# Kernel optimization log

Measured on AMD Instinct MI355X. Metric: run time of the kernel, lower is better.

The kernel has to match this reference:

```python
import jax, jax.numpy as jnp
import numpy as np

N = 48
E = N * (N - 1)
H_LSTM = 32
EPS = 20.0

def _conv1d(x, w, b):
    # x: [B, Cin, L], w: [Cout, Cin, K] -> [B, Cout, L], 'same' padding
    y = jax.lax.conv_general_dilated(x, w, window_strides=(1,), padding='SAME',
                                     dimension_numbers=('NCH', 'OIH', 'NCH'))
    return y + b[None, :, None]

def _map(M, x):
    # map_features: linear map along dim 0 (gather for n_to_e one-hot rows,
    # incidence-sum scatter for e_to_n). M: [O, I], x: [I, ...] -> [O, ...]
    return jnp.tensordot(M, x, axes=1)

def _node_cnn(x, adj, layers, final):
    # graph conv stack: neighbor mix (adj along dim 0) + conv1d over node axis + relu
    nl = len(layers)
    for i, (w, b) in enumerate(layers):
        x = _conv1d(_map(adj, x), w, b)
        if not (final and i == nl - 1):
            x = jax.nn.relu(x)
    return x

def _node_lstm(x, mem, adj, w, b):
    # mem = cat([c, h], dim=1); gates from conv over adj-mixed cat([x, h])
    H = mem.shape[1] // 2
    c, h = mem[:, :H], mem[:, H:]
    gates = _conv1d(_map(adj, jnp.concatenate([x, h], axis=1)), w, b)
    i, f, g, o = jnp.split(gates, 4, axis=1)
    c2 = jax.nn.sigmoid(f) * c + jax.nn.sigmoid(i) * jnp.tanh(g)
    h2 = jax.nn.sigmoid(o) * jnp.tanh(c2)
    return jnp.concatenate([c2, h2], axis=1)

def _forward(bi, bij, msgi, msgj, v, nmem0, emem0, neadj, eeadj,
             e_to_n0, e_to_n1, n_to_e0, n_to_e1, decoding, params):
    fm, efm, nlstm, elstm, pp, epp = params
    n = bi.shape[0]
    e = bij.shape[0]
    # map_node_feature_to_edge
    bi_g1 = _map(n_to_e0, bi)   # [E,1,N]
    bi_g2 = _map(n_to_e1, bi)   # [E,1,N]
    # softmax (logsumexp) message computation over bij [E,1,N,N]
    cmsgi = jax.nn.logsumexp((bi_g2[:, :, None, :] + bij) * EPS, axis=3) / EPS  # [E,1,N]
    cmsgj = jax.nn.logsumexp((bi_g1[:, :, :, None] + bij) * EPS, axis=2) / EPS  # [E,1,N]
    ncmsgi = _map(e_to_n0, cmsgi)
    ncmsgj = _map(e_to_n1, cmsgj)
    nnmsgi = _map(e_to_n0, msgi)
    nnmsgj = _map(e_to_n1, msgj)
    # partial_feature (detached in original)
    dec_mat = jax.nn.one_hot(decoding, n, dtype=bi.dtype)        # [N,N]
    xi = _map(n_to_e0, dec_mat)[:, :, None]                      # [E,N,1]
    xj = _map(n_to_e1, dec_mat)[:, None, :]                      # [E,1,N]
    ep = bij.reshape(e, n, n)
    f1 = jax.lax.stop_gradient(_map(e_to_n0, (ep * xi).sum(axis=1)).reshape(n, 1, n))
    f2 = jax.lax.stop_gradient(_map(e_to_n1, (ep * xj).sum(axis=2)).reshape(n, 1, n))
    node_feature = jnp.concatenate([bi, bi + v, nnmsgi, nnmsgj, ncmsgi, ncmsgj, f1, f2], axis=1)  # [N,8,N]
    edge_feature = jnp.concatenate([msgi, msgj, cmsgi, cmsgj, bi_g1, bi_g2], axis=1)              # [E,6,N]
    nfeat = _node_cnn(node_feature, neadj, fm, False)   # [N,32,N]
    efeat = _node_cnn(edge_feature, eeadj, efm, False)  # [E,32,N]
    ntoe1, ntoe2 = _map(n_to_e0, nfeat), _map(n_to_e1, nfeat)
    eton1, eton2 = _map(e_to_n0, efeat), _map(e_to_n1, efeat)
    nfeat = jnp.concatenate([nfeat, eton1, eton2], axis=1)  # [N,96,N]
    efeat = jnp.concatenate([efeat, ntoe1, ntoe2], axis=1)  # [E,96,N]
    nmem_new = _node_lstm(nfeat, nmem0, neadj, nlstm[0], nlstm[1])  # [N,64,N]
    emem_new = _node_lstm(efeat, emem0, eeadj, elstm[0], elstm[1])  # [E,64,N]
    nfeat = nmem_new[:, H_LSTM:]   # h part
    efeat = emem_new[:, H_LSTM:]
    ntoe1, ntoe2 = _map(n_to_e0, nfeat), _map(n_to_e1, nfeat)
    eton1, eton2 = _map(e_to_n0, efeat), _map(e_to_n1, efeat)
    nfeat = jnp.concatenate([nfeat, eton1, eton2], axis=1)
    efeat = jnp.concatenate([efeat, ntoe1, ntoe2], axis=1)
    efeat = _node_cnn(efeat, eeadj, epp, True)   # [E,2,N]
    nfeat = _node_cnn(nfeat, neadj, pp, True)    # [N,1,N]
    nmsgi = efeat[:, 0:1] + 0.5 * cmsgi - msgi
    nmsgj = efeat[:, 1:2] + 0.5 * cmsgj - msgj
    nv = nfeat.mean(axis=0, keepdims=True)       # [1,1,N]
    v_out = v + nv
    bij_out = bij - nmsgi.reshape(e, 1, n, 1) - nmsgj.reshape(e, 1, 1, n)
    bi_out = bi + _map(e_to_n0, nmsgi) + _map(e_to_n1, nmsgj) - nv
    msgi_out = msgi + nmsgi
    msgj_out = msgj + nmsgj
    # get_current_dual (softmax=True)
    cdual = (v_out.sum()
             + jax.nn.logsumexp(bi_out.reshape(-1, n) * EPS, axis=1).sum() / EPS
             + jax.nn.logsumexp(bij_out.reshape(-1, n * n) * EPS, axis=1).sum() / EPS)
    return bi_out, bij_out, msgi_out, msgj_out, v_out, cdual, nmem_new, emem_new, f1, f2

def setup_inputs() -> dict:
    key = jax.random.key(0)
    ks = jax.random.split(key, 16)
    ii, jj = np.meshgrid(np.arange(N), np.arange(N), indexing='ij')
    mask = ii != jj
    src, dst = ii[mask], jj[mask]  # [E] complete directed graph
    eye = np.eye(N, dtype=np.float32)
    n_to_e0 = jnp.asarray(eye[src])  # [E,N] one-hot gather
    n_to_e1 = jnp.asarray(eye[dst])
    e_to_n0 = n_to_e0.T              # [N,E] incidence scatter-sum
    e_to_n1 = n_to_e1.T
    def glorot(k, shape):
        fan_in = shape[1] * shape[2]
        return jax.random.normal(k, shape, jnp.float32) / np.sqrt(fan_in)
    pk = jax.random.split(ks[15], 20)
    return dict(
        bi=jax.random.normal(ks[0], (N, 1, N), jnp.float32),
        bij=jax.random.normal(ks[1], (E, 1, N, N), jnp.float32),
        msgi=jnp.zeros((E, 1, N), jnp.float32),
        msgj=jnp.zeros((E, 1, N), jnp.float32),
        v=jnp.zeros((1, 1, N), jnp.float32),
        nmem0=jnp.zeros((N, 2 * H_LSTM, N), jnp.float32),
        emem0=jnp.zeros((E, 2 * H_LSTM, N), jnp.float32),
        neadj=jax.random.uniform(ks[2], (N, N), jnp.float32) / N,
        eeadj=jax.random.uniform(ks[3], (E, E), jnp.float32) / E,
        e_to_n0=e_to_n0, e_to_n1=e_to_n1, n_to_e0=n_to_e0, n_to_e1=n_to_e1,
        decoding=jax.random.randint(ks[4], (N,), 0, N),
        fm_w0=glorot(pk[0], (32, 8, 3)), fm_b0=jnp.zeros((32,), jnp.float32),
        fm_w1=glorot(pk[1], (32, 32, 3)), fm_b1=jnp.zeros((32,), jnp.float32),
        efm_w0=glorot(pk[2], (32, 6, 3)), efm_b0=jnp.zeros((32,), jnp.float32),
        efm_w1=glorot(pk[3], (32, 32, 3)), efm_b1=jnp.zeros((32,), jnp.float32),
        nlstm_w=glorot(pk[4], (128, 128, 3)), nlstm_b=jnp.zeros((128,), jnp.float32),
        elstm_w=glorot(pk[5], (128, 128, 3)), elstm_b=jnp.zeros((128,), jnp.float32),
        pp_w0=glorot(pk[6], (16, 96, 3)), pp_b0=jnp.zeros((16,), jnp.float32),
        pp_w1=glorot(pk[7], (1, 16, 3)), pp_b1=jnp.zeros((1,), jnp.float32),
        epp_w0=glorot(pk[8], (16, 96, 3)), epp_b0=jnp.zeros((16,), jnp.float32),
        epp_w1=glorot(pk[9], (2, 16, 3)), epp_b1=jnp.zeros((2,), jnp.float32),
    )

def reference(bi, bij, msgi, msgj, v, nmem0, emem0, neadj, eeadj,
              e_to_n0, e_to_n1, n_to_e0, n_to_e1, decoding,
              fm_w0, fm_b0, fm_w1, fm_b1, efm_w0, efm_b0, efm_w1, efm_b1,
              nlstm_w, nlstm_b, elstm_w, elstm_b,
              pp_w0, pp_b0, pp_w1, pp_b1, epp_w0, epp_b0, epp_w1, epp_b1):
    params = ([(fm_w0, fm_b0), (fm_w1, fm_b1)],
              [(efm_w0, efm_b0), (efm_w1, efm_b1)],
              (nlstm_w, nlstm_b), (elstm_w, elstm_b),
              [(pp_w0, pp_b0), (pp_w1, pp_b1)],
              [(epp_w0, epp_b0), (epp_w1, epp_b1)])
    return _forward(bi, bij, msgi, msgj, v, nmem0, emem0, neadj, eeadj,
                    e_to_n0, e_to_n1, n_to_e0, n_to_e1, decoding, params)
```

## Files before the change

kernel.cpp:

```cpp
#include <hip/hip_runtime.h>
#include <cstdint>
#include <cstddef>

#define EE 2256
#define EP 2304

typedef __attribute__((ext_vector_type(8))) short bf16x8;
typedef __attribute__((ext_vector_type(4))) float f32x4;

__device__ __forceinline__ unsigned short f2b(float f){
  unsigned u = __builtin_bit_cast(unsigned, f);
  u += 0x7fffu + ((u>>16)&1u);
  return (unsigned short)(u>>16);
}
__device__ __forceinline__ float b2f(unsigned short h){
  unsigned u = ((unsigned)h)<<16; return __builtin_bit_cast(float, u);
}
__device__ __forceinline__ float sigm(float x){ return 1.f/(1.f+__expf(-x)); }
__device__ __forceinline__ float tanhfast(float x){ return 1.f - 2.f/(__expf(2.f*x)+1.f); }

__device__ __forceinline__ int xcd_swz(int bid, int nwg){
  int xcd = bid & 7, idx = bid >> 3;
  int q = nwg >> 3, r = nwg & 7;
  return (xcd < r ? xcd*(q+1) : r*(q+1) + (xcd-r)*q) + idx;
// ... 80 lines not shown
                              float* ncmi, float* ncmj, float* nnmi, float* nnmj,
                              float* o_f1, float* o_f2){
  int i = blockIdx.x; int tid = threadIdx.x;
  __shared__ float red[5][6][48];
  int mg = tid / 48;
  int w  = tid - mg*48;
  if (mg < 5){
    int dc = dec[i];
    float a1=0,a2=0,a3=0,a4=0,s1=0,s2=0;
    for (int m=mg; m<47; m+=5){
      int e1 = i*47+m;
      a1 += cmi[e1*48+w]; a3 += msgi[e1*48+w];
      s1 += bij[(size_t)e1*2304 + dc*48 + w];
      int j = m + (m>=i); int e2 = j*47 + i - (i>j);
      a2 += cmj[e2*48+w]; a4 += msgj[e2*48+w];
      s2 += bij[(size_t)e2*2304 + w*48 + dc];
    }
    red[mg][0][w]=a1; red[mg][1][w]=a2; red[mg][2][w]=a3;
    red[mg][3][w]=a4; red[mg][4][w]=s1; red[mg][5][w]=s2;
  }
  __syncthreads();
  if (tid < 48){
    float a1=0,a2=0,a3=0,a4=0,s1=0,s2=0;
    for (int g=0; g<5; g++){
      a1+=red[g][0][tid]; a2+=red[g][1][tid]; a3+=red[g][2][tid];
      a4+=red[g][3][tid]; s1+=red[g][4][tid]; s2+=red[g][5][tid];
    }
    ncmi[i*48+tid]=a1; ncmj[i*48+tid]=a2; nnmi[i*48+tid]=a3; nnmj[i*48+tid]=a4;
    o_f1[i*48+tid]=s1; o_f2[i*48+tid]=s2;
  }
}

__global__ void gm_build_x6(const float* __restrict__ msgi, const float* __restrict__ msgj,
                            const float* __restrict__ cmi, const float* __restrict__ cmj,
                            const float* __restrict__ bi, unsigned short* __restrict__ x6){
  int idx = blockIdx.x*256 + threadIdx.x;
  if (idx >= 288*EP) return;
  int row = idx / EP, e = idx - row*EP;
  int w = row / 6, c = row - w*6;
  unsigned short val = 0;
  if (e < EE){
    int s = e/47, m = e-s*47, d = m + (m>=s);
    float x;
    switch(c){
      case 0: x = msgi[e*48+w]; break;
      case 1: x = msgj[e*48+w]; break;
      case 2: x = cmi[e*48+w]; break;
      case 3: x = cmj[e*48+w]; break;
      case 4: x = bi[s*48+w]; break;
      default: x = bi[d*48+w]; break;
    }
    val = f2b(x);
  }
  x6[idx] = val;
}

__global__ void gm_fill_x128_hi(const float* __restrict__ emem0, const float* __restrict__ nfeat,
                                unsigned short* __restrict__ x128){
  int idx = blockIdx.x*256 + threadIdx.x;
  if (idx >= 96*EP) return;
  int q = idx/EP; int c = 32 + q; int e = idx - q*EP;
  if (e >= EE){ for (int w=0;w<48;w++) x128[(size_t)(w*128+c)*EP + e] = 0; return; }
  int s=e/47, m=e-s*47, d=m+(m>=s);
  const float* srcrow;
  if (c < 64)      srcrow = nfeat + ((size_t)s*32 + (c-32))*48;
  else if (c < 96) srcrow = nfeat + ((size_t)d*32 + (c-64))*48;
  else             srcrow = emem0 + ((size_t)e*64 + (c-64))*48;
  #pragma unroll
  for (int w4=0; w4<12; w4++){
    float4 xv = *(const float4*)(srcrow + w4*4);
    x128[(size_t)((w4*4+0)*128+c)*EP + e] = f2b(xv.x);
    x128[(size_t)((w4*4+1)*128+c)*EP + e] = f2b(xv.y);
    x128[(size_t)((w4*4+2)*128+c)*EP + e] = f2b(xv.z);
    x128[(size_t)((w4*4+3)*128+c)*EP + e] = f2b(xv.w);
  }
}

__global__ __launch_bounds__(256) void gm_map_gemm(
    const unsigned short* __restrict__ A, const unsigned short* __restrict__ BT,
    unsigned short* __restrict__ ypad, float* __restrict__ outf,
    const float* __restrict__ bias, int nrow, int Nvalid, int Cch, int Cslab,
    int do_relu, int f32_out)
{
  __shared__ __align__(16) unsigned short lA[2][128*32];
  __shared__ __align__(16) unsigned short lB[2][128*32];
  const int tid = threadIdx.x;
  const int lane = tid & 63, wid = tid >> 6;
  const int swz = xcd_swz(blockIdx.x, gridDim.x);
  const int m0 = (swz % nrow) * 128;
  const int n0 = (swz / nrow) * 128;
  const int wm = wid >> 1, wn = wid & 1;
  f32x4 acc[4][4];
  #pragma unroll
  for (int i=0;i<4;i++){
    #pragma unroll
    for (int j=0;j<4;j++) acc[i][j] = f32x4{0.f,0.f,0.f,0.f};
  }
  const int srow = (lane>>2), scol = (lane&3);

  auto STAGE = [&](int ks, int b){
    #pragma unroll
    for (int q=0;q<2;q++){
      int chunk = wid*2+q;
      int row = chunk*16 + srow;
      int off = (scol*16) ^ (((row>>1)&3)<<4);
      glds16((const char*)A  + (size_t)(m0+row)*(EP*2) + ks*64 + off, (char*)lA[b] + chunk*1024);
      glds16((const char*)BT + (size_t)(n0+row)*(EP*2) + ks*64 + off, (char*)lB[b] + chunk*1024);
    }
  };
  auto COMPUTE = [&](int b){
    bf16x8 af[4], bfr[4];
    #pragma unroll
    for (int mi=0;mi<4;mi++){
      int row = wm*64 + mi*16 + (lane&15);
      int off = ((lane>>4)*16) ^ (((row>>1)&3)<<4);
      af[mi] = *(const bf16x8*)((const char*)lA[b] + row*64 + off);
    }
    #pragma unroll
    for (int ni=0;ni<4;ni++){
      int row = wn*64 + ni*16 + (lane&15);
      int off = ((lane>>4)*16) ^ (((row>>1)&3)<<4);
      bfr[ni] = *(const bf16x8*)((const char*)lB[b] + row*64 + off);
    }
    #pragma unroll
    for (int mi=0;mi<4;mi++){
      #pragma unroll
      for (int ni=0;ni<4;ni++)
        acc[mi][ni] = __builtin_amdgcn_mfma_f32_16x16x32_bf16(af[mi], bfr[ni], acc[mi][ni], 0,0,0);
    }
  };

  STAGE(0, 0);
  __syncthreads();
  int cur = 0;
  for (int ks = 0; ks < EP/32; ++ks){
    if (ks+1 < EP/32) STAGE(ks+1, cur^1);
    COMPUTE(cur);
    __syncthreads();
    cur ^= 1;
  }
  #pragma unroll
  for (int mi=0;mi<4;mi++){
    int ebase = m0 + wm*64 + mi*16 + (lane>>4)*4;
    #pragma unroll
    for (int ni=0;ni<4;ni++){
      int c = n0 + wn*64 + ni*16 + (lane&15);
      if (c >= Nvalid) continue;
      int w = c / Cch, ci = c - w*Cch;
      float bv = bias ? bias[ci] : 0.f;
      #pragma unroll
      for (int r=0;r<4;r++){
        int e = ebase + r;
        if (e >= EE) continue;
        float x = acc[mi][ni][r] + bv;
        if (do_relu) x = fmaxf(x, 0.f);
        if (f32_out) outf[(size_t)e*Nvalid + c] = x;
        else ypad[((size_t)e*50 + 1 + w)*Cslab + ci] = f2b(x);
      }
    }
  }
}

__global__ __launch_bounds__(256) void gm_map_sk(
    const unsigned short* __restrict__ A, const unsigned short* __restrict__ BT,
    float* __restrict__ pbuf, int nrow, int ncol, int S, int kspan)
{
  __shared__ __align__(16) unsigned short lA[2][128*32];
  __shared__ __align__(16) unsigned short lB[2][128*32];
  const int tid = threadIdx.x;
  const int lane = tid & 63, wid = tid >> 6;
  const int swz = xcd_swz(blockIdx.x, gridDim.x);
  const int ntile = nrow*ncol;
  const int sp = swz / ntile;
  const int tile = swz - sp*ntile;
  const int m0 = (tile % nrow) * 128;
  const int n0 = (tile / nrow) * 128;
  const int Npad = ncol*128;
  const int k0 = sp*kspan, k1 = k0 + kspan;
  const int wm = wid >> 1, wn = wid & 1;
  f32x4 acc[4][4];
  #pragma unroll
  for (int i=0;i<4;i++){
    #pragma unroll
    for (int j=0;j<4;j++) acc[i][j] = f32x4{0.f,0.f,0.f,0.f};
  }
  const int srow = (lane>>2), scol = (lane&3);

  auto STAGE = [&](int ks, int b){
    #pragma unroll
    for (int q=0;q<2;q++){
      int chunk = wid*2+q;
      int row = chunk*16 + srow;
      int off = (scol*16) ^ (((row>>1)&3)<<4);
      glds16((const char*)A  + (size_t)(m0+row)*(EP*2) + ks*64 + off, (char*)lA[b] + chunk*1024);
      glds16((const char*)BT + (size_t)(n0+row)*(EP*2) + ks*64 + off, (char*)lB[b] + chunk*1024);
    }
  };
  auto COMPUTE = [&](int b){
    bf16x8 af[4], bfr[4];
    #pragma unroll
    for (int mi=0;mi<4;mi++){
      int row = wm*64 + mi*16 + (lane&15);
      int off = ((lane>>4)*16) ^ (((row>>1)&3)<<4);
      af[mi] = *(const bf16x8*)((const char*)lA[b] + row*64 + off);
    }
    #pragma unroll
    for (int ni=0;ni<4;ni++){
      int row = wn*64 + ni*16 + (lane&15);
      int off = ((lane>>4)*16) ^ (((row>>1)&3)<<4);
      bfr[ni] = *(const bf16x8*)((const char*)lB[b] + row*64 + off);
    }
    #pragma unroll
    for (int mi=0;mi<4;mi++){
      #pragma unroll
      for (int ni=0;ni<4;ni++)
        acc[mi][ni] = __builtin_amdgcn_mfma_f32_16x16x32_bf16(af[mi], bfr[ni], acc[mi][ni], 0,0,0);
    }
  };

  STAGE(k0, 0);
  __syncthreads();
  int cur = 0;
  for (int ks = k0; ks < k1; ++ks){
    if (ks+1 < k1) STAGE(ks+1, cur^1);
    COMPUTE(cur);
    __syncthreads();
    cur ^= 1;
  }
  float* pb = pbuf + (size_t)sp*2304*Npad;
  #pragma unroll
  for (int mi=0;mi<4;mi++){
    int ebase = m0 + wm*64 + mi*16 + (lane>>4)*4;
    #pragma unroll
    for (int ni=0;ni<4;ni++){
      int c = n0 + wn*64 + ni*16 + (lane&15);
      #pragma unroll
      for (int r=0;r<4;r++)
        pb[(size_t)(ebase+r)*Npad + c] = acc[mi][ni][r];
    }
  }
}

__global__ void gm_sk_fin(const float* __restrict__ pbuf, unsigned short* __restrict__ ypad,
                          float* __restrict__ outf, const float* __restrict__ bias,
                          int S, int Npad, int Nvalid, int Cch, int Cslab, int do_relu, int f32_out){
  int idx = blockIdx.x*256 + threadIdx.x;
  if (idx >= EE*Nvalid) return;
  int e = idx / Nvalid, c = idx - e*Nvalid;
  float s = 0.f;
  for (int p=0;p<S;p++) s += pbuf[(size_t)p*2304*Npad + (size_t)e*Npad + c];
  int w = c / Cch, ci = c - w*Cch;
  if (bias) s += bias[ci];
  if (do_relu) s = fmaxf(s, 0.f);
  if (f32_out) outf[(size_t)e*Nvalid + c] = s;
  else ypad[((size_t)e*50 + 1 + w)*Cslab + ci] = f2b(s);
}

template<int BM>
__global__ __launch_bounds__(256) void gm_conv_gemm(
    const unsigned short* __restrict__ Wp, const unsigned short* __restrict__ ypad,
    unsigned short* __restrict__ outT, const float* __restrict__ bias,
    int Cch, int KPT, int Kpad, int Co, int Ct, int do_relu)
{
  constexpr int MI = (BM==128)?4:((BM==32)?2:1);
  constexpr int NI = (BM==128)?4:2;
  __shared__ __align__(16) unsigned short lA[2][BM*32];
  __shared__ __align__(16) unsigned short lB[2][128*32];
  const int tid = threadIdx.x, lane = tid&63, wid = tid>>6;
  const int swz = xcd_swz(blockIdx.x, 864);
  const int e0 = (swz / 48) * 128;
  const int w  = swz % 48;
  const int rowb = (BM==128)? (wid>>1)*64 : 0;
  const int colb = (BM==128)? (wid&1)*64 : wid*32;
  f32x4 acc[MI][NI];
  #pragma unroll
  for (int i=0;i<MI;i++){
    #pragma unroll
    for (int j=0;j<NI;j++) acc[i][j] = f32x4{0.f,0.f,0.f,0.f};
  }
  const int srow=(lane>>2), scol=(lane&3);
  const int ksteps = Kpad/32;

  auto STAGE = [&](int ks, int b){
    for (int c = wid; c < BM/16; c += 4){
      int row = c*16 + srow;
      int off = (scol*16) ^ (((row>>1)&3)<<4);
      glds16((const char*)Wp + (size_t)row*(Kpad*2) + ks*64 + off, (char*)lA[b] + c*1024);
    }
    for (int c = wid; c < 8; c += 4){
      int row = c*16 + srow;
      int off = (scol*16) ^ (((row>>1)&3)<<4);
      int kg = ks*32 + (off>>1);
      int t = kg / KPT;
      int ci = kg - t*KPT;
      int e = e0 + row;
      const char* src;
      if (t < 3 && e < EE) src = (const char*)ypad + ((size_t)(e*50 + w + t)*Cch + ci)*2;
      else                 src = (const char*)ypad;
      glds16(src, (char*)lB[b] + c*1024);
    }
  };
  auto COMPUTE = [&](int b){
    bf16x8 af[MI], bfr[NI];
    #pragma unroll
    for (int mi=0;mi<MI;mi++){
      int row = rowb + mi*16 + (lane&15);
      int off = ((lane>>4)*16) ^ (((row>>1)&3)<<4);
      af[mi] = *(const bf16x8*)((const char*)lA[b] + row*64 + off);
    }
    #pragma unroll
    for (int ni=0;ni<NI;ni++){
      int row = colb + ni*16 + (lane&15);
      int off = ((lane>>4)*16) ^ (((row>>1)&3)<<4);
      bfr[ni] = *(const bf16x8*)((const char*)lB[b] + row*64 + off);
    }
    #pragma unroll
    for (int mi=0;mi<MI;mi++){
      #pragma unroll
      for (int ni=0;ni<NI;ni++)
        acc[mi][ni] = __builtin_amdgcn_mfma_f32_16x16x32_bf16(af[mi], bfr[ni], acc[mi][ni], 0,0,0);
    }
  };

  STAGE(0, 0);
  __syncthreads();
  int cur = 0;
  for (int ks=0; ks<ksteps; ++ks){
    if (ks+1 < ksteps) STAGE(ks+1, cur^1);
    COMPUTE(cur);
    __syncthreads();
    cur ^= 1;
  }
  #pragma unroll
  for (int mi=0;mi<MI;mi++){
    #pragma unroll
    for (int ni=0;ni<NI;ni++){
      int m = colb + ni*16 + (lane&15);
      int e = e0 + m;
      if (e >= EE) continue;
      #pragma unroll
      for (int r=0;r<4;r++){
        int co = rowb + mi*16 + (lane>>4)*4 + r;
        if (co >= Co) continue;
        float x = acc[mi][ni][r] + (bias ? bias[co] : 0.f);
        if (do_relu) x = fmaxf(x, 0.f);
        outT[((size_t)(w*Ct + co))*EP + e] = f2b(x);
      }
    }
  }
}

__global__ void gm_build_nf(const float* __restrict__ bi, const float* __restrict__ v,
                            const float* __restrict__ nnmi, const float* __restrict__ nnmj,
                            const float* __restrict__ ncmi, const float* __restrict__ ncmj,
                            const float* __restrict__ f1, const float* __restrict__ f2,
                            float* __restrict__ nf){
  int idx = blockIdx.x*256+threadIdx.x;
  if (idx >= 48*8*48) return;
  int i = idx/(8*48); int rem = idx - i*(8*48); int c = rem/48; int w = rem-c*48;
  int iw = i*48+w;
  float x;
  switch(c){
    case 0: x=bi[iw]; break;
    case 1: x=bi[iw]+v[w]; break;
    case 2: x=nnmi[iw]; break;
    case 3: x=nnmj[iw]; break;
    case 4: x=ncmi[iw]; break;
    case 5: x=ncmj[iw]; break;
    case 6: x=f1[iw]; break;
    default: x=f2[iw]; break;
  }
  nf[idx]=x;
}

__global__ void gm_nmap(const float* __restrict__ adj, const float* __restrict__ X,
                        float* __restrict__ Y, int C){
  int idx = blockIdx.x*256 + threadIdx.x;
  int tot = 48*C*48;
  if (idx >= tot) return;
  int i = idx/(C*48); int rem = idx - i*(C*48);
  float s=0.f;
  for (int j=0;j<48;j++) s += adj[i*48+j]*X[(size_t)j*C*48 + rem];
  Y[idx]=s;
}

__global__ void gm_nconv(const float* __restrict__ X, const float* __restrict__ wgt,
                         const float* __restrict__ bias, float* __restrict__ Y,
                         int Cin, int Co, int relu){
  int idx = blockIdx.x*256 + threadIdx.x;
  int tot = 48*Co*48;
  if (idx >= tot) return;
  int i = idx/(Co*48); int rem = idx - i*(Co*48); int co = rem/48; int w = rem-co*48;
  float s = bias[co];
  const float* xb = X + (size_t)i*Cin*48;
  const float* wb = wgt + (size_t)co*Cin*3;
  for (int ci=0; ci<Cin; ++ci){
    float w0 = wb[ci*3], w1 = wb[ci*3+1], w2 = wb[ci*3+2];
    const float* xr = xb + ci*48;
    if (w > 0) s += xr[w-1]*w0;
    s += xr[w]*w1;
    if (w < 47) s += xr[w+1]*w2;
  }
  if (relu) s = fmaxf(s, 0.f);
  Y[idx] = s;
}

__global__ __launch_bounds__(256) void gm_nconv_lstm(const float* __restrict__ X,
    const float* __restrict__ wgt, const float* __restrict__ bias,
    const float* __restrict__ nmem0, float* __restrict__ o_nmem, float* __restrict__ nfeat2){
  int idx = blockIdx.x*256 + threadIdx.x;
  if (idx >= 48*32*48) return;
  int i = idx/(32*48); int rem = idx - i*(32*48); int ch = rem/48; int w = rem-ch*48;
  const float* xb = X + (size_t)i*128*48;
  float s0=bias[ch], s1=bias[32+ch], s2=bias[64+ch], s3=bias[96+ch];
  for (int ci=0; ci<128; ++ci){
    const float* xr = xb + ci*48;
    float xm = (w>0)? xr[w-1] : 0.f;
    float xc = xr[w];
    float xp = (w<47)? xr[w+1] : 0.f;
    const float* wb0 = wgt + ((size_t)ch*128+ci)*3;
    const float* wb1 = wgt + ((size_t)(32+ch)*128+ci)*3;
    const float* wb2 = wgt + ((size_t)(64+ch)*128+ci)*3;
    const float* wb3 = wgt + ((size_t)(96+ch)*128+ci)*3;
    s0 += xm*wb0[0]+xc*wb0[1]+xp*wb0[2];
    s1 += xm*wb1[0]+xc*wb1[1]+xp*wb1[2];
    s2 += xm*wb2[0]+xc*wb2[1]+xp*wb2[2];
    s3 += xm*wb3[0]+xc*wb3[1]+xp*wb3[2];
  }
  float c = nmem0[((size_t)i*64+ch)*48+w];
  float c2 = sigm(s1)*c + sigm(s0)*tanhfast(s2);
  float h2 = sigm(s3)*tanhfast(c2);
  o_nmem[((size_t)i*64+ch)*48+w] = c2;
  o_nmem[((size_t)i*64+32+ch)*48+w] = h2;
  nfeat2[((size_t)i*32+ch)*48+w] = h2;
}

__global__ __launch_bounds__(256) void gm_eton_x128(const unsigned short* __restrict__ x128,
                                                    float* __restrict__ xn){
  int row = blockIdx.x;
  int w = row >> 5, cc = row & 31;
  __shared__ float L[2256];
  const unsigned short* src = x128 + (size_t)(w*128 + cc)*EP;
  for (int t=threadIdx.x; t<2256; t+=256) L[t] = b2f(src[t]);
  __syncthreads();
  int tid = threadIdx.x;
  if (tid < 48){
    int i = tid; float s=0.f;
    for (int m=0;m<47;m++) s += L[i*47+m];
    xn[((size_t)i*128 + 32 + cc)*48 + w] = s;
  } else if (tid >= 64 && tid < 112){
    int i = tid-64; float s=0.f;
    for (int m=0;m<47;m++){
      int j = m + (m>=i);
      s += L[j*47 + i - (i>j)];
    }
    xn[((size_t)i*128 + 64 + cc)*48 + w] = s;
  }
}

__global__ void gm_xnode_copy(const float* __restrict__ nfeat, const float* __restrict__ nmem0,
                              float* __restrict__ xn){
  int idx = blockIdx.x*256+threadIdx.x;
  if (idx >= 48*64*48) return;
  int i = idx/(64*48); int rem = idx - i*(64*48); int c = rem/48; int w = rem-c*48;
  if (c < 32) xn[((size_t)i*128 + c)*48 + w] = nfeat[((size_t)i*32+c)*48+w];
  else        xn[((size_t)i*128 + 96 + (c-32))*48 + w] = nmem0[((size_t)i*64 + 32 + (c-32))*48 + w];
}

__global__ __launch_bounds__(256) void gm_elstm_pw(const unsigned short* __restrict__ gatesT,
                                                   const float* __restrict__ emem0,
                                                   float* __restrict__ o_emem){
  int bid = blockIdx.x;
  int e4 = bid / 6, chunk = bid - e4*6;
  int cw = chunk*256 + threadIdx.x;
  int ch = cw / 48, w = cw - ch*48;
  int ebase = e4*4;
  const unsigned short* g0 = gatesT + (size_t)(w*128 + ch)*EP + ebase;
  ushort4 vi = *(const ushort4*)(g0);
  ushort4 vf = *(const ushort4*)(g0 + (size_t)32*EP);
  ushort4 vg = *(const ushort4*)(g0 + (size_t)64*EP);
  ushort4 vo = *(const ushort4*)(g0 + (size_t)96*EP);
  const unsigned short* pi = (const unsigned short*)&vi;
  const unsigned short* pf = (const unsigned short*)&vf;
  const unsigned short* pg = (const unsigned short*)&vg;
  const unsigned short* po = (const unsigned short*)&vo;
  #pragma unroll
  for (int r=0;r<4;r++){
    int e = ebase + r;
    float gi = b2f(pi[r]), gf = b2f(pf[r]), gg = b2f(pg[r]), go = b2f(po[r]);
    float c  = emem0[((size_t)e*64 + ch)*48 + w];
    float c2 = sigm(gf)*c + sigm(gi)*tanhfast(gg);
    float h2 = sigm(go)*tanhfast(c2);
    o_emem[((size_t)e*64 + ch)*48 + w] = c2;
    o_emem[((size_t)e*64 + 32+ch)*48 + w] = h2;
  }
}

__global__ __launch_bounds__(256) void gm_eton_h(const float* __restrict__ o_emem,
                                                 float* __restrict__ x2){
  int row = blockIdx.x; int w = row >> 5, cc = row & 31;
  __shared__ float L[2256];
  for (int t=threadIdx.x; t<2256; t+=256)
    L[t] = o_emem[((size_t)t*64 + 32 + cc)*48 + w];
  __syncthreads();
  int tid = threadIdx.x;
  if (tid < 48){
    int i=tid; float s=0.f;
    for (int m=0;m<47;m++) s += L[i*47+m];
    x2[((size_t)i*96 + 32 + cc)*48 + w] = s;
  } else if (tid>=64 && tid<112){
    int i=tid-64; float s=0.f;
    for (int m=0;m<47;m++){ int j=m+(m>=i); s += L[j*47 + i - (i>j)]; }
    x2[((size_t)i*96 + 64 + cc)*48 + w] = s;
  }
}

__global__ void gm_x2_copy(const float* __restrict__ nfeat2, float* __restrict__ x2){
// ... 69 lines not shown
    float x = src[idx] - ri[r] - rj[c];
    dst[idx] = x; v[q] = x; mx = fmaxf(mx, x);
  }
  for (int o=1;o<64;o<<=1) mx = fmaxf(mx, __shfl_xor(mx, o, 64));
  int lane = tid&63, w4 = tid>>6;
  if (lane==0) red[w4] = mx;
  __syncthreads();
  mx = fmaxf(fmaxf(red[0],red[1]),fmaxf(red[2],red[3]));
  float s = 0.f;
  #pragma unroll
  for (int q=0;q<9;q++) s += __expf((v[q]-mx)*20.f);
  for (int o=1;o<64;o<<=1) s += __shfl_xor(s, o, 64);
  if (lane==0) red[4+w4] = s;
  __syncthreads();
  if (tid==0){
    float t = red[4]+red[5]+red[6]+red[7];
    lse_e[e] = mx + __logf(t)*(1.f/20.f);
  }
}

__global__ void gm_biout(const float* __restrict__ bi, const float* __restrict__ nmi,
                         const float* __restrict__ nmj, const float* __restrict__ nv,
                         float* __restrict__ o_bi, float* __restrict__ lse_n){
  int i = blockIdx.x; int w = threadIdx.x;
  float val = -1e30f;
  if (w < 48){
    float s = 0.f;
    for (int m=0;m<47;m++){
      int e1 = i*47+m;
      s += nmi[e1*48+w];
      int j = m + (m>=i);
      int e2 = j*47 + i - (i>j);
      s += nmj[e2*48+w];
    }
    val = bi[i*48+w] + s - nv[w];
    o_bi[i*48+w] = val;
  }
  float mx = val;
  for (int o=1;o<64;o<<=1) mx = fmaxf(mx, __shfl_xor(mx, o, 64));
  float ex = (w<48)? __expf((val-mx)*20.f) : 0.f;
  for (int o=1;o<64;o<<=1) ex += __shfl_xor(ex, o, 64);
  if (w==0) lse_n[i] = mx + __logf(ex)*(1.f/20.f);
}

__global__ void gm_cdual(const float* __restrict__ lse_e, const float* __restrict__ lse_n,
                         const float* __restrict__ vout, float* __restrict__ out){
  int tid = threadIdx.x;
  float s = 0.f;
  for (int i=tid;i<EE;i+=256) s += lse_e[i];
  if (tid<48) s += lse_n[tid] + vout[tid];
  __shared__ float red[4];
  for (int o=1;o<64;o<<=1) s += __shfl_xor(s,o,64);
  if ((tid&63)==0) red[tid>>6]=s;
  __syncthreads();
  if (tid==0) out[0] = red[0]+red[1]+red[2]+red[3];
}

static constexpr size_t A256v(size_t x){ return (x+255)&~(size_t)255; }
static constexpr size_t OFF_EEADJ = 0;
static constexpr size_t OFF_X6T   = A256v(OFF_EEADJ + (size_t)EP*EP*2);
static constexpr size_t OFF_X32T  = A256v(OFF_X6T  + (size_t)384*EP*2);
static constexpr size_t OFF_X128T = A256v(OFF_X32T + (size_t)1536*EP*2);
static constexpr size_t OFF_YP6   = A256v(OFF_X128T + (size_t)6144*EP*2);
static constexpr size_t OFF_YP32  = A256v(OFF_YP6  + (size_t)EE*50*8*2);
static constexpr size_t OFF_YP128 = A256v(OFF_YP32 + (size_t)EE*50*32*2);
static constexpr size_t OFF_YP16  = A256v(OFF_YP128 + (size_t)EE*50*128*2);
static constexpr size_t OFF_ZEND  = A256v(OFF_YP16 + (size_t)EE*50*16*2 + 256);
static constexpr size_t OFF_XPP   = OFF_YP128;
static constexpr size_t OFF_SKP   = OFF_YP128;
static constexpr size_t OFF_WC0 = OFF_ZEND;
static constexpr size_t OFF_WC1 = A256v(OFF_WC0 + 32*32*2);
static constexpr size_t OFF_WCL = A256v(OFF_WC1 + 32*96*2);
static constexpr size_t OFF_WP0 = A256v(OFF_WCL + 128*384*2);
static constexpr size_t OFF_WP1 = A256v(OFF_WP0 + 16*288*2);
static constexpr size_t OFF_CMI = A256v(OFF_WP1 + 16*64*2);
static constexpr size_t OFF_CMJ = A256v(OFF_CMI + (size_t)EE*48*4);
static constexpr size_t OFF_NMI = A256v(OFF_CMJ + (size_t)EE*48*4);
static constexpr size_t OFF_NMJ = A256v(OFF_NMI + (size_t)EE*48*4);
static constexpr size_t OFF_EFPP= A256v(OFF_NMJ + (size_t)EE*48*4);
static constexpr size_t OFF_LSEE= A256v(OFF_EFPP + (size_t)EE*96*4);
static constexpr size_t OFF_LSEN= A256v(OFF_LSEE + EE*4);
static constexpr size_t OFF_NV  = A256v(OFF_LSEN + 48*4);
static constexpr size_t OFF_NF  = A256v(OFF_NV + 48*4);
static constexpr size_t OFF_NT1 = A256v(OFF_NF + (size_t)48*8*48*4);
static constexpr size_t OFF_NT2 = A256v(OFF_NT1 + (size_t)48*128*48*4);
static constexpr size_t OFF_NFEAT = A256v(OFF_NT2 + (size_t)48*128*48*4);
static constexpr size_t OFF_NFEAT2= A256v(OFF_NFEAT + (size_t)48*32*48*4);
static constexpr size_t OFF_XN  = A256v(OFF_NFEAT2 + (size_t)48*32*48*4);
static constexpr size_t OFF_NFPP= A256v(OFF_XN + (size_t)48*128*48*4);
static constexpr size_t OFF_NAC = A256v(OFF_NFPP + (size_t)48*48*4);

extern "C" void kernel_launch(void* const* d_in, const int* in_sizes, int n_in,
                              void* d_out, int out_size, void* d_ws, size_t ws_size,
                              hipStream_t stream) {
  const float* bi    = (const float*)d_in[0];
  const float* bij   = (const float*)d_in[1];
  const float* msgi  = (const float*)d_in[2];
  const float* msgj  = (const float*)d_in[3];
  const float* v_in  = (const float*)d_in[4];
  const float* nmem0 = (const float*)d_in[5];
  const float* emem0 = (const float*)d_in[6];
  const float* neadj = (const float*)d_in[7];
  const float* eeadj = (const float*)d_in[8];
  const int*   dec   = (const int*)d_in[13];
  const float* fm_w0 = (const float*)d_in[14]; const float* fm_b0 = (const float*)d_in[15];
  const float* fm_w1 = (const float*)d_in[16]; const float* fm_b1 = (const float*)d_in[17];
  const float* efm_w0= (const float*)d_in[18]; const float* efm_b0= (const float*)d_in[19];
  const float* efm_w1= (const float*)d_in[20]; const float* efm_b1= (const float*)d_in[21];
  const float* nl_w  = (const float*)d_in[22]; const float* nl_b  = (const float*)d_in[23];
  const float* el_w  = (const float*)d_in[24]; const float* el_b  = (const float*)d_in[25];
  const float* pp_w0 = (const float*)d_in[26]; const float* pp_b0 = (const float*)d_in[27];
  const float* pp_w1 = (const float*)d_in[28]; const float* pp_b1 = (const float*)d_in[29];
  const float* epp_w0= (const float*)d_in[30]; const float* epp_b0= (const float*)d_in[31];
  const float* epp_w1= (const float*)d_in[32]; const float* epp_b1= (const float*)d_in[33];

  char* ws = (char*)d_ws;
  unsigned short* eeadjb = (unsigned short*)(ws + OFF_EEADJ);
  unsigned short* x6t    = (unsigned short*)(ws + OFF_X6T);
  unsigned short* x32t   = (unsigned short*)(ws + OFF_X32T);
  unsigned short* x128t  = (unsigned short*)(ws + OFF_X128T);
  unsigned short* z1t    = x32t;
  unsigned short* z2t    = x6t;
  unsigned short* gatesT = x128t;
  unsigned short* yp6    = (unsigned short*)(ws + OFF_YP6);
  unsigned short* yp32   = (unsigned short*)(ws + OFF_YP32);
  unsigned short* yp128  = (unsigned short*)(ws + OFF_YP128);
  unsigned short* yp16   = (unsigned short*)(ws + OFF_YP16);
  unsigned short* xpp    = (unsigned short*)(ws + OFF_XPP);
  float*          skp    = (float*)(ws + OFF_SKP);
  unsigned short* wc0 = (unsigned short*)(ws + OFF_WC0);
  unsigned short* wc1 = (unsigned short*)(ws + OFF_WC1);
  unsigned short* wcl = (unsigned short*)(ws + OFF_WCL);
  unsigned short* wp0 = (unsigned short*)(ws + OFF_WP0);
  unsigned short* wp1 = (unsigned short*)(ws + OFF_WP1);
  float* cmi  = (float*)(ws + OFF_CMI);
  float* cmj  = (float*)(ws + OFF_CMJ);
  float* nmi  = (float*)(ws + OFF_NMI);
  float* nmj  = (float*)(ws + OFF_NMJ);
  float* effpp= (float*)(ws + OFF_EFPP);
  float* lse_e= (float*)(ws + OFF_LSEE);
  float* lse_n= (float*)(ws + OFF_LSEN);
  float* nvb  = (float*)(ws + OFF_NV);
  float* nf   = (float*)(ws + OFF_NF);
  float* nt1  = (float*)(ws + OFF_NT1);
  float* nt2  = (float*)(ws + OFF_NT2);
  float* nfeat  = (float*)(ws + OFF_NFEAT);
  float* nfeat2 = (float*)(ws + OFF_NFEAT2);
  float* xn   = (float*)(ws + OFF_XN);
  float* nfpp = (float*)(ws + OFF_NFPP);
  float* ncmi = (float*)(ws + OFF_NAC);
  float* ncmj = ncmi + 2304;
  float* nnmi = ncmi + 2*2304;
  float* nnmj = ncmi + 3*2304;

  float* out = (float*)d_out;
  float* o_bi   = out;
  float* o_bij  = out + 2304;
  float* o_mi   = out + 2304 + 5197824;
  float* o_mj   = o_mi + 108288;
  float* o_v    = o_mj + 108288;
  float* o_cd   = o_v + 48;
  float* o_nmem = o_cd + 1;
  float* o_emem = o_nmem + 147456;
  float* o_f1   = o_emem + 6930432;
  float* o_f2   = o_f1 + 2304;

  gm_zero_pads<<<EE, 128, 0, stream>>>(yp6, yp32, yp16);
  gm_prep_eeadj<<<(EP*EP+255)/256, 256, 0, stream>>>(eeadj, eeadjb);
  gm_prep_wall<<<(58880+255)/256, 256, 0, stream>>>(efm_w0, efm_w1, el_w, epp_w0, epp_w1,
                                                    wc0, wc1, wcl, wp0, wp1);
  gm_cmsg<<<EE, 128, 0, stream>>>(bi, bij, cmi, cmj);
  gm_node_accum<<<48, 256, 0, stream>>>(bij, cmi, cmj, msgi, msgj, dec, ncmi, ncmj, nnmi, nnmj, o_f1, o_f2);
  gm_build_x6<<<(288*EP+255)/256, 256, 0, stream>>>(msgi, msgj, cmi, cmj, bi, x6t);
  gm_build_nf<<<(48*8*48+255)/256, 256, 0, stream>>>(bi, v_in, nnmi, nnmj, ncmi, ncmj, o_f1, o_f2, nf);
  gm_nmap<<<(48*8*48+255)/256, 256, 0, stream>>>(neadj, nf, nt1, 8);
  gm_nconv<<<(48*32*48+255)/256, 256, 0, stream>>>(nt1, fm_w0, fm_b0, nt2, 8, 32, 1);
  gm_nmap<<<(48*32*48+255)/256, 256, 0, stream>>>(neadj, nt2, nt1, 32);
  gm_nconv<<<(48*32*48+255)/256, 256, 0, stream>>>(nt1, fm_w1, fm_b1, nfeat, 32, 32, 1);
  gm_map_sk<<<216, 256, 0, stream>>>(eeadjb, x6t, skp, 18, 3, 4, 18);
  gm_sk_fin<<<(EE*288+255)/256, 256, 0, stream>>>(skp, yp6, nullptr, nullptr, 4, 384, 288, 6, 8, 0, 0);
  gm_conv_gemm<32><<<864, 256, 0, stream>>>(wc0, yp6,  x32t, efm_b0, 8, 8, 32, 32, 32, 1);
  gm_map_gemm<<<216, 256, 0, stream>>>(eeadjb, x32t, yp32, nullptr, nullptr, 18, 1536, 32, 32, 0, 0);
  gm_conv_gemm<32><<<864, 256, 0, stream>>>(wc1, yp32, x128t, efm_b1, 32, 32, 96, 32, 128, 1);
  gm_fill_x128_hi<<<(96*EP+255)/256, 256, 0, stream>>>(emem0, nfeat, x128t);
  gm_xnode_copy<<<(48*64*48+255)/256, 256, 0, stream>>>(nfeat, nmem0, xn);
  gm_eton_x128<<<1536, 256, 0, stream>>>(x128t, xn);
  gm_nmap<<<(48*128*48+255)/256, 256, 0, stream>>>(neadj, xn, nt1, 128);
  gm_nconv_lstm<<<(48*32*48+255)/256, 256, 0, stream>>>(nt1, nl_w, nl_b, nmem0, o_nmem, nfeat2);
  gm_zero_pad128<<<EE, 128, 0, stream>>>(yp128);
  gm_map_gemm<<<864, 256, 0, stream>>>(eeadjb, x128t, yp128, nullptr, nullptr, 18, 6144, 128, 128, 0, 0);
  gm_conv_gemm<128><<<864, 256, 0, stream>>>(wcl, yp128, gatesT, el_b, 128, 128, 384, 128, 128, 0);
  gm_elstm_pw<<<564*6, 256, 0, stream>>>(gatesT, emem0, o_emem);
  gm_build_xpp<<<EE, 128, 0, stream>>>(o_emem, nfeat2, xpp);
  gm_conv_gemm<16><<<864, 256, 0, stream>>>(wp0, xpp,  z1t, nullptr, 96, 96, 288, 16, 16, 0);
  gm_map_sk<<<432, 256, 0, stream>>>(eeadjb, z1t, skp, 18, 6, 4, 18);
  gm_sk_fin<<<(EE*768+255)/256, 256, 0, stream>>>(skp, yp16, nullptr, epp_b0, 4, 768, 768, 16, 16, 1, 0);
  gm_conv_gemm<16><<<864, 256, 0, stream>>>(wp1, yp16, z2t, nullptr, 16, 16, 64, 2, 2, 0);
  gm_map_sk<<<144, 256, 0, stream>>>(eeadjb, z2t, skp, 18, 1, 8, 9);
  gm_sk_fin<<<(EE*96+255)/256, 256, 0, stream>>>(skp, nullptr, effpp, epp_b1, 8, 128, 96, 2, 2, 0, 1);
  gm_x2_copy<<<(48*32*48+255)/256, 256, 0, stream>>>(nfeat2, xn);
  gm_eton_h<<<1536, 256, 0, stream>>>(o_emem, xn);
  gm_nmap<<<(48*96*48+255)/256, 256, 0, stream>>>(neadj, xn, nt1, 96);
  gm_nconv<<<(48*16*48+255)/256, 256, 0, stream>>>(nt1, pp_w0, pp_b0, nt2, 96, 16, 1);
  gm_nmap<<<(48*16*48+255)/256, 256, 0, stream>>>(neadj, nt2, nt1, 16);
  gm_nconv<<<(48*1*48+255)/256, 256, 0, stream>>>(nt1, pp_w1, pp_b1, nfpp, 16, 1, 0);
  gm_nv<<<1, 64, 0, stream>>>(nfpp, v_in, nvb, o_v);
  gm_bijout<<<EE, 256, 0, stream>>>(bij, effpp, cmi, cmj, msgi, msgj, nmi, nmj, o_mi, o_mj, o_bij, lse_e);
  gm_biout<<<48, 64, 0, stream>>>(bi, nmi, nmj, nvb, o_bi, lse_n);
  gm_cdual<<<1, 256, 0, stream>>>(lse_e, lse_n, o_v, o_cd);
}
```

Before: 811.7 us.

## Single-buffer LDS in GEMM kernels and fuse node map+conv into one kernel

Removes double-buffered LDS staging from the three MFMA GEMM kernels. They now load a tile, sync, compute and sync each k-step, which halves shared memory per block but stops overlapping loads with compute. It also fuses the node adjacency mix and conv1d (including the node LSTM) into per-node kernels that keep the mixed tile in shared memory. This drops five launches and the global intermediate buffer, but runs only 48 blocks.

```diff
diff --git a/kernel.cpp b/kernel.cpp
--- a/kernel.cpp
+++ b/kernel.cpp
@@ -186,8 +186,8 @@
     const float* __restrict__ bias, int nrow, int Nvalid, int Cch, int Cslab,
     int do_relu, int f32_out)
 {
-  __shared__ __align__(16) unsigned short lA[2][128*32];
-  __shared__ __align__(16) unsigned short lB[2][128*32];
+  __shared__ __align__(16) unsigned short lA[128*32];
+  __shared__ __align__(16) unsigned short lB[128*32];
   const int tid = threadIdx.x;
   const int lane = tid & 63, wid = tid >> 6;
   const int swz = xcd_swz(blockIdx.x, gridDim.x);
@@ -202,29 +202,28 @@
   }
   const int srow = (lane>>2), scol = (lane&3);
 
-  auto STAGE = [&](int ks, int b){
+  for (int ks = 0; ks < EP/32; ++ks) {
     #pragma unroll
     for (int q=0;q<2;q++){
       int chunk = wid*2+q;
       int row = chunk*16 + srow;
       int off = (scol*16) ^ (((row>>1)&3)<<4);
-      glds16((const char*)A  + (size_t)(m0+row)*(EP*2) + ks*64 + off, (char*)lA[b] + chunk*1024);
-      glds16((const char*)BT + (size_t)(n0+row)*(EP*2) + ks*64 + off, (char*)lB[b] + chunk*1024);
-    }
-  };
-  auto COMPUTE = [&](int b){
+      glds16((const char*)A  + (size_t)(m0+row)*(EP*2) + ks*64 + off, (char*)lA + chunk*1024);
+      glds16((const char*)BT + (size_t)(n0+row)*(EP*2) + ks*64 + off, (char*)lB + chunk*1024);
+    }
+    __syncthreads();
     bf16x8 af[4], bfr[4];
     #pragma unroll
     for (int mi=0;mi<4;mi++){
       int row = wm*64 + mi*16 + (lane&15);
       int off = ((lane>>4)*16) ^ (((row>>1)&3)<<4);
-      af[mi] = *(const bf16x8*)((const char*)lA[b] + row*64 + off);
+      af[mi] = *(const bf16x8*)((const char*)lA + row*64 + off);
     }
     #pragma unroll
     for (int ni=0;ni<4;ni++){
       int row = wn*64 + ni*16 + (lane&15);
       int off = ((lane>>4)*16) ^ (((row>>1)&3)<<4);
-      bfr[ni] = *(const bf16x8*)((const char*)lB[b] + row*64 + off);
+      bfr[ni] = *(const bf16x8*)((const char*)lB + row*64 + off);
     }
     #pragma unroll
     for (int mi=0;mi<4;mi++){
@@ -232,16 +231,7 @@
       for (int ni=0;ni<4;ni++)
         acc[mi][ni] = __builtin_amdgcn_mfma_f32_16x16x32_bf16(af[mi], bfr[ni], acc[mi][ni], 0,0,0);
     }
-  };
-
-  STAGE(0, 0);
-  __syncthreads();
-  int cur = 0;
-  for (int ks = 0; ks < EP/32; ++ks){
-    if (ks+1 < EP/32) STAGE(ks+1, cur^1);
-    COMPUTE(cur);
     __syncthreads();
-    cur ^= 1;
   }
   #pragma unroll
   for (int mi=0;mi<4;mi++){
@@ -269,8 +259,8 @@
     const unsigned short* __restrict__ A, const unsigned short* __restrict__ BT,
     float* __restrict__ pbuf, int nrow, int ncol, int S, int kspan)
 {
-  __shared__ __align__(16) unsigned short lA[2][128*32];
-  __shared__ __align__(16) unsigned short lB[2][128*32];
+  __shared__ __align__(16) unsigned short lA[128*32];
+  __shared__ __align__(16) unsigned short lB[128*32];
   const int tid = threadIdx.x;
   const int lane = tid & 63, wid = tid >> 6;
   const int swz = xcd_swz(blockIdx.x, gridDim.x);
@@ -290,29 +280,28 @@
   }
   const int srow = (lane>>2), scol = (lane&3);
 
-  auto STAGE = [&](int ks, int b){
+  for (int ks = k0; ks < k1; ++ks){
     #pragma unroll
     for (int q=0;q<2;q++){
       int chunk = wid*2+q;
       int row = chunk*16 + srow;
       int off = (scol*16) ^ (((row>>1)&3)<<4);
-      glds16((const char*)A  + (size_t)(m0+row)*(EP*2) + ks*64 + off, (char*)lA[b] + chunk*1024);
-      glds16((const char*)BT + (size_t)(n0+row)*(EP*2) + ks*64 + off, (char*)lB[b] + chunk*1024);
-    }
-  };
-  auto COMPUTE = [&](int b){
+      glds16((const char*)A  + (size_t)(m0+row)*(EP*2) + ks*64 + off, (char*)lA + chunk*1024);
+      glds16((const char*)BT + (size_t)(n0+row)*(EP*2) + ks*64 + off, (char*)lB + chunk*1024);
+    }
+    __syncthreads();
     bf16x8 af[4], bfr[4];
     #pragma unroll
     for (int mi=0;mi<4;mi++){
       int row = wm*64 + mi*16 + (lane&15);
       int off = ((lane>>4)*16) ^ (((row>>1)&3)<<4);
-      af[mi] = *(const bf16x8*)((const char*)lA[b] + row*64 + off);
+      af[mi] = *(const bf16x8*)((const char*)lA + row*64 + off);
     }
     #pragma unroll
     for (int ni=0;ni<4;ni++){
       int row = wn*64 + ni*16 + (lane&15);
       int off = ((lane>>4)*16) ^ (((row>>1)&3)<<4);
-      bfr[ni] = *(const bf16x8*)((const char*)lB[b] + row*64 + off);
+      bfr[ni] = *(const bf16x8*)((const char*)lB + row*64 + off);
     }
     #pragma unroll
     for (int mi=0;mi<4;mi++){
@@ -320,16 +309,7 @@
       for (int ni=0;ni<4;ni++)
         acc[mi][ni] = __builtin_amdgcn_mfma_f32_16x16x32_bf16(af[mi], bfr[ni], acc[mi][ni], 0,0,0);
     }
-  };
-
-  STAGE(k0, 0);
-  __syncthreads();
-  int cur = 0;
-  for (int ks = k0; ks < k1; ++ks){
-    if (ks+1 < k1) STAGE(ks+1, cur^1);
-    COMPUTE(cur);
     __syncthreads();
-    cur ^= 1;
   }
   float* pb = pbuf + (size_t)sp*2304*Npad;
   #pragma unroll
@@ -368,8 +348,8 @@
 {
   constexpr int MI = (BM==128)?4:((BM==32)?2:1);
   constexpr int NI = (BM==128)?4:2;
-  __shared__ __align__(16) unsigned short lA[2][BM*32];
-  __shared__ __align__(16) unsigned short lB[2][128*32];
+  __shared__ __align__(16) unsigned short lA[BM*32];
+  __shared__ __align__(16) unsigned short lB[128*32];
   const int tid = threadIdx.x, lane = tid&63, wid = tid>>6;
   const int swz = xcd_swz(blockIdx.x, 864);
   const int e0 = (swz / 48) * 128;
@@ -384,12 +364,11 @@
   }
   const int srow=(lane>>2), scol=(lane&3);
   const int ksteps = Kpad/32;
-
-  auto STAGE = [&](int ks, int b){
+  for (int ks=0; ks<ksteps; ++ks){
     for (int c = wid; c < BM/16; c += 4){
       int row = c*16 + srow;
       int off = (scol*16) ^ (((row>>1)&3)<<4);
-      glds16((const char*)Wp + (size_t)row*(Kpad*2) + ks*64 + off, (char*)lA[b] + c*1024);
+      glds16((const char*)Wp + (size_t)row*(Kpad*2) + ks*64 + off, (char*)lA + c*1024);
     }
     for (int c = wid; c < 8; c += 4){
       int row = c*16 + srow;
@@ -401,22 +380,21 @@
       const char* src;
       if (t < 3 && e < EE) src = (const char*)ypad + ((size_t)(e*50 + w + t)*Cch + ci)*2;
       else                 src = (const char*)ypad;
-      glds16(src, (char*)lB[b] + c*1024);
-    }
-  };
-  auto COMPUTE = [&](int b){
+      glds16(src, (char*)lB + c*1024);
+    }
+    __syncthreads();
     bf16x8 af[MI], bfr[NI];
     #pragma unroll
     for (int mi=0;mi<MI;mi++){
       int row = rowb + mi*16 + (lane&15);
       int off = ((lane>>4)*16) ^ (((row>>1)&3)<<4);
-      af[mi] = *(const bf16x8*)((const char*)lA[b] + row*64 + off);
+      af[mi] = *(const bf16x8*)((const char*)lA + row*64 + off);
     }
     #pragma unroll
     for (int ni=0;ni<NI;ni++){
       int row = colb + ni*16 + (lane&15);
       int off = ((lane>>4)*16) ^ (((row>>1)&3)<<4);
-      bfr[ni] = *(const bf16x8*)((const char*)lB[b] + row*64 + off);
+      bfr[ni] = *(const bf16x8*)((const char*)lB + row*64 + off);
     }
     #pragma unroll
     for (int mi=0;mi<MI;mi++){
@@ -424,16 +402,7 @@
       for (int ni=0;ni<NI;ni++)
         acc[mi][ni] = __builtin_amdgcn_mfma_f32_16x16x32_bf16(af[mi], bfr[ni], acc[mi][ni], 0,0,0);
     }
-  };
-
-  STAGE(0, 0);
-  __syncthreads();
-  int cur = 0;
-  for (int ks=0; ks<ksteps; ++ks){
-    if (ks+1 < ksteps) STAGE(ks+1, cur^1);
-    COMPUTE(cur);
     __syncthreads();
-    cur ^= 1;
   }
   #pragma unroll
   for (int mi=0;mi<MI;mi++){
@@ -477,66 +446,76 @@
   nf[idx]=x;
 }
 
-__global__ void gm_nmap(const float* __restrict__ adj, const float* __restrict__ X,
-                        float* __restrict__ Y, int C){
-  int idx = blockIdx.x*256 + threadIdx.x;
-  int tot = 48*C*48;
-  if (idx >= tot) return;
-  int i = idx/(C*48); int rem = idx - i*(C*48);
-  float s=0.f;
-  for (int j=0;j<48;j++) s += adj[i*48+j]*X[(size_t)j*C*48 + rem];
-  Y[idx]=s;
-}
-
-__global__ void gm_nconv(const float* __restrict__ X, const float* __restrict__ wgt,
-                         const float* __restrict__ bias, float* __restrict__ Y,
-                         int Cin, int Co, int relu){
-  int idx = blockIdx.x*256 + threadIdx.x;
-  int tot = 48*Co*48;
-  if (idx >= tot) return;
-  int i = idx/(Co*48); int rem = idx - i*(Co*48); int co = rem/48; int w = rem-co*48;
-  float s = bias[co];
-  const float* xb = X + (size_t)i*Cin*48;
-  const float* wb = wgt + (size_t)co*Cin*3;
-  for (int ci=0; ci<Cin; ++ci){
-    float w0 = wb[ci*3], w1 = wb[ci*3+1], w2 = wb[ci*3+2];
-    const float* xr = xb + ci*48;
-    if (w > 0) s += xr[w-1]*w0;
-    s += xr[w]*w1;
-    if (w < 47) s += xr[w+1]*w2;
-  }
-  if (relu) s = fmaxf(s, 0.f);
-  Y[idx] = s;
-}
-
-__global__ __launch_bounds__(256) void gm_nconv_lstm(const float* __restrict__ X,
-    const float* __restrict__ wgt, const float* __restrict__ bias,
+__global__ __launch_bounds__(256) void gm_mapconv(const float* __restrict__ adj,
+    const float* __restrict__ X, const float* __restrict__ wgt, const float* __restrict__ bias,
+    float* __restrict__ Y, int Cin, int Co, int relu){
+  int i = blockIdx.x;
+  __shared__ float t[96*48];
+  __shared__ float arow[48];
+  int tid = threadIdx.x;
+  if (tid < 48) arow[tid] = adj[i*48+tid];
+  __syncthreads();
+  for (int cw = tid; cw < Cin*48; cw += 256){
+    float s = 0.f;
+    for (int j=0;j<48;j++) s += arow[j] * X[(size_t)j*Cin*48 + cw];
+    t[cw] = s;
+  }
+  __syncthreads();
+  for (int cow = tid; cow < Co*48; cow += 256){
+    int co = cow/48, w = cow-co*48;
+    float s = bias[co];
+    const float* wb = wgt + (size_t)co*Cin*3;
+    for (int ci=0; ci<Cin; ++ci){
+      const float* xr = t + ci*48;
+      float w0=wb[ci*3], w1=wb[ci*3+1], w2=wb[ci*3+2];
+      if (w>0) s += xr[w-1]*w0;
+      s += xr[w]*w1;
+      if (w<47) s += xr[w+1]*w2;
+    }
+    if (relu) s = fmaxf(s,0.f);
+    Y[(size_t)i*Co*48 + cow] = s;
+  }
+}
+
+__global__ __launch_bounds__(512) void gm_mapconv_lstm(const float* __restrict__ adj,
+    const float* __restrict__ X, const float* __restrict__ wgt, const float* __restrict__ bias,
     const float* __restrict__ nmem0, float* __restrict__ o_nmem, float* __restrict__ nfeat2){
-  int idx = blockIdx.x*256 + threadIdx.x;
-  if (idx >= 48*32*48) return;
-  int i = idx/(32*48); int rem = idx - i*(32*48); int ch = rem/48; int w = rem-ch*48;
-  const float* xb = X + (size_t)i*128*48;
-  float s0=bias[ch], s1=bias[32+ch], s2=bias[64+ch], s3=bias[96+ch];
-  for (int ci=0; ci<128; ++ci){
-    const float* xr = xb + ci*48;
-    float xm = (w>0)? xr[w-1] : 0.f;
-    float xc = xr[w];
-    float xp = (w<47)? xr[w+1] : 0.f;
-    const float* wb0 = wgt + ((size_t)ch*128+ci)*3;
-    const float* wb1 = wgt + ((size_t)(32+ch)*128+ci)*3;
-    const float* wb2 = wgt + ((size_t)(64+ch)*128+ci)*3;
-    const float* wb3 = wgt + ((size_t)(96+ch)*128+ci)*3;
-    s0 += xm*wb0[0]+xc*wb0[1]+xp*wb0[2];
-    s1 += xm*wb1[0]+xc*wb1[1]+xp*wb1[2];
-    s2 += xm*wb2[0]+xc*wb2[1]+xp*wb2[2];
-    s3 += xm*wb3[0]+xc*wb3[1]+xp*wb3[2];
-  }
-  float c = nmem0[((size_t)i*64+ch)*48+w];
-  float c2 = sigm(s1)*c + sigm(s0)*tanhfast(s2);
-  float h2 = sigm(s3)*tanhfast(c2);
-  o_nmem[((size_t)i*64+ch)*48+w] = c2;
-  o_nmem[((size_t)i*64+32+ch)*48+w] = h2;
-  nfeat2[((size_t)i*32+ch)*48+w] = h2;
+  int i = blockIdx.x;
+  __shared__ float t[128*48];
+  __shared__ float arow[48];
+  int tid = threadIdx.x;
+  if (tid < 48) arow[tid] = adj[i*48+tid];
+  __syncthreads();
+  for (int cw = tid; cw < 128*48; cw += 512){
+    float s = 0.f;
+    for (int j=0;j<48;j++) s += arow[j] * X[(size_t)j*6144 + cw];
+    t[cw] = s;
+  }
+  __syncthreads();
+  for (int chw = tid; chw < 32*48; chw += 512){
+    int ch = chw/48, w = chw-ch*48;
+    float s0=bias[ch], s1=bias[32+ch], s2=bias[64+ch], s3=bias[96+ch];
+    for (int ci=0; ci<128; ++ci){
+      const float* xr = t + ci*48;
+      float xm = (w>0)? xr[w-1] : 0.f;
+      float xc = xr[w];
+      float xp = (w<47)? xr[w+1] : 0.f;
+      const float* wb0 = wgt + ((size_t)ch*128+ci)*3;
+      const float* wb1 = wgt + ((size_t)(32+ch)*128+ci)*3;
+      const float* wb2 = wgt + ((size_t)(64+ch)*128+ci)*3;
+      const float* wb3 = wgt + ((size_t)(96+ch)*128+ci)*3;
+      s0 += xm*wb0[0]+xc*wb0[1]+xp*wb0[2];
+      s1 += xm*wb1[0]+xc*wb1[1]+xp*wb1[2];
+      s2 += xm*wb2[0]+xc*wb2[1]+xp*wb2[2];
+      s3 += xm*wb3[0]+xc*wb3[1]+xp*wb3[2];
+    }
+    float c = nmem0[((size_t)i*64+ch)*48+w];
+    float c2 = sigm(s1)*c + sigm(s0)*tanhfast(s2);
+    float h2 = sigm(s3)*tanhfast(c2);
+    o_nmem[((size_t)i*64+ch)*48+w] = c2;
+    o_nmem[((size_t)i*64+32+ch)*48+w] = h2;
+    nfeat2[((size_t)i*32+ch)*48+w] = h2;
+  }
 }
 
 __global__ __launch_bounds__(256) void gm_eton_x128(const unsigned short* __restrict__ x128,
@@ -772,9 +751,8 @@
 static constexpr size_t OFF_LSEN= A256v(OFF_LSEE + EE*4);
 static constexpr size_t OFF_NV  = A256v(OFF_LSEN + 48*4);
 static constexpr size_t OFF_NF  = A256v(OFF_NV + 48*4);
-static constexpr size_t OFF_NT1 = A256v(OFF_NF + (size_t)48*8*48*4);
-static constexpr size_t OFF_NT2 = A256v(OFF_NT1 + (size_t)48*128*48*4);
-static constexpr size_t OFF_NFEAT = A256v(OFF_NT2 + (size_t)48*128*48*4);
+static constexpr size_t OFF_NT2 = A256v(OFF_NF + (size_t)48*8*48*4);
+static constexpr size_t OFF_NFEAT = A256v(OFF_NT2 + (size_t)48*32*48*4);
 static constexpr size_t OFF_NFEAT2= A256v(OFF_NFEAT + (size_t)48*32*48*4);
 static constexpr size_t OFF_XN  = A256v(OFF_NFEAT2 + (size_t)48*32*48*4);
 static constexpr size_t OFF_NFPP= A256v(OFF_XN + (size_t)48*128*48*4);
@@ -832,7 +810,6 @@
   float* lse_n= (float*)(ws + OFF_LSEN);
   float* nvb  = (float*)(ws + OFF_NV);
   float* nf   = (float*)(ws + OFF_NF);
-  float* nt1  = (float*)(ws + OFF_NT1);
   float* nt2  = (float*)(ws + OFF_NT2);
   float* nfeat  = (float*)(ws + OFF_NFEAT);
   float* nfeat2 = (float*)(ws + OFF_NFEAT2);
@@ -863,10 +840,8 @@
   gm_node_accum<<<48, 256, 0, stream>>>(bij, cmi, cmj, msgi, msgj, dec, ncmi, ncmj, nnmi, nnmj, o_f1, o_f2);
   gm_build_x6<<<(288*EP+255)/256, 256, 0, stream>>>(msgi, msgj, cmi, cmj, bi, x6t);
   gm_build_nf<<<(48*8*48+255)/256, 256, 0, stream>>>(bi, v_in, nnmi, nnmj, ncmi, ncmj, o_f1, o_f2, nf);
-  gm_nmap<<<(48*8*48+255)/256, 256, 0, stream>>>(neadj, nf, nt1, 8);
-  gm_nconv<<<(48*32*48+255)/256, 256, 0, stream>>>(nt1, fm_w0, fm_b0, nt2, 8, 32, 1);
-  gm_nmap<<<(48*32*48+255)/256, 256, 0, stream>>>(neadj, nt2, nt1, 32);
-  gm_nconv<<<(48*32*48+255)/256, 256, 0, stream>>>(nt1, fm_w1, fm_b1, nfeat, 32, 32, 1);
+  gm_mapconv<<<48, 256, 0, stream>>>(neadj, nf,  fm_w0, fm_b0, nt2,   8, 32, 1);
+  gm_mapconv<<<48, 256, 0, stream>>>(neadj, nt2, fm_w1, fm_b1, nfeat, 32, 32, 1);
   gm_map_sk<<<216, 256, 0, stream>>>(eeadjb, x6t, skp, 18, 3, 4, 18);
   gm_sk_fin<<<(EE*288+255)/256, 256, 0, stream>>>(skp, yp6, nullptr, nullptr, 4, 384, 288, 6, 8, 0, 0);
   gm_conv_gemm<32><<<864, 256, 0, stream>>>(wc0, yp6,  x32t, efm_b0, 8, 8, 32, 32, 32, 1);
@@ -875,8 +850,7 @@
   gm_fill_x128_hi<<<(96*EP+255)/256, 256, 0, stream>>>(emem0, nfeat, x128t);
   gm_xnode_copy<<<(48*64*48+255)/256, 256, 0, stream>>>(nfeat, nmem0, xn);
   gm_eton_x128<<<1536, 256, 0, stream>>>(x128t, xn);
-  gm_nmap<<<(48*128*48+255)/256, 256, 0, stream>>>(neadj, xn, nt1, 128);
-  gm_nconv_lstm<<<(48*32*48+255)/256, 256, 0, stream>>>(nt1, nl_w, nl_b, nmem0, o_nmem, nfeat2);
+  gm_mapconv_lstm<<<48, 512, 0, stream>>>(neadj, xn, nl_w, nl_b, nmem0, o_nmem, nfeat2);
   gm_zero_pad128<<<EE, 128, 0, stream>>>(yp128);
   gm_map_gemm<<<864, 256, 0, stream>>>(eeadjb, x128t, yp128, nullptr, nullptr, 18, 6144, 128, 128, 0, 0);
   gm_conv_gemm<128><<<864, 256, 0, stream>>>(wcl, yp128, gatesT, el_b, 128, 128, 384, 128, 128, 0);
@@ -890,10 +864,8 @@
   gm_sk_fin<<<(EE*96+255)/256, 256, 0, stream>>>(skp, nullptr, effpp, epp_b1, 8, 128, 96, 2, 2, 0, 1);
   gm_x2_copy<<<(48*32*48+255)/256, 256, 0, stream>>>(nfeat2, xn);
   gm_eton_h<<<1536, 256, 0, stream>>>(o_emem, xn);
-  gm_nmap<<<(48*96*48+255)/256, 256, 0, stream>>>(neadj, xn, nt1, 96);
-  gm_nconv<<<(48*16*48+255)/256, 256, 0, stream>>>(nt1, pp_w0, pp_b0, nt2, 96, 16, 1);
-  gm_nmap<<<(48*16*48+255)/256, 256, 0, stream>>>(neadj, nt2, nt1, 16);
-  gm_nconv<<<(48*1*48+255)/256, 256, 0, stream>>>(nt1, pp_w1, pp_b1, nfpp, 16, 1, 0);
+  gm_mapconv<<<48, 256, 0, stream>>>(neadj, xn,  pp_w0, pp_b0, nt2, 96, 16, 1);
+  gm_mapconv<<<48, 256, 0, stream>>>(neadj, nt2, pp_w1, pp_b1, nfpp, 16, 1, 0);
   gm_nv<<<1, 64, 0, stream>>>(nfpp, v_in, nvb, o_v);
   gm_bijout<<<EE, 256, 0, stream>>>(bij, effpp, cmi, cmj, msgi, msgj, nmi, nmj, o_mi, o_mj, o_bij, lse_e);
   gm_biout<<<48, 64, 0, stream>>>(bi, nmi, nmj, nvb, o_bi, lse_n);
```

Result: slower. 1.008 ms (+24.2%).
